# Optimization experiments

Measured on AMD Instinct MI355X. Metric: run time of the kernel, lower is better.

The kernel has to match this reference:

```python
import jax, jax.numpy as jnp
import numpy as np

N_CLUSTER = 1
SIZE, RATIO = 32, 0.1


def _lin_mat(n_in, n_out):
    # bilinear, align_corners=True interpolation matrix [n_out, n_in]
    src = np.arange(n_out) * (n_in - 1) / (n_out - 1)
    lo = np.floor(src).astype(np.int64)
    hi = np.minimum(lo + 1, n_in - 1)
    w = (src - lo).astype(np.float32)
    M = np.zeros((n_out, n_in), np.float32)
    M[np.arange(n_out), lo] += 1.0 - w
    M[np.arange(n_out), hi] += w
    return jnp.asarray(M)


def setup_inputs() -> dict:
    key = jax.random.key(0)
    ks = jax.random.split(key, 5)
    B, D, H, W, C = 16, 128, 128, 128, 6
    inp = {
        "assp": jax.random.normal(ks[0], (B, D, H, W), jnp.float32),
        "cls_w": jax.random.normal(ks[1], (C, D), jnp.float32) * 0.05,
        "cls_b": jnp.zeros((C,), jnp.float32),
        "key_w": jax.random.normal(ks[2], (128, D), jnp.float32) * 0.05,
        "key_b": jnp.zeros((128,), jnp.float32),
        "query_w": jax.random.normal(ks[3], (C, 128, D), jnp.float32) * 0.05,
        "query_b": jnp.zeros((C, 128), jnp.float32),
    }
    rng = np.random.default_rng(0)
    idx = rng.permutation(SIZE * SIZE)[: int(SIZE * SIZE * RATIO)]  # 102 unique pixels
    inp["px"] = jnp.asarray(idx // SIZE, jnp.int32)
    inp["py"] = jnp.asarray(idx % SIZE, jnp.int32)
    return inp


def reference(assp, cls_w, cls_b, key_w, key_b, query_w, query_b, px, py):
    B, D, H, W = assp.shape
    C = cls_w.shape[0]
    # pseudo labels (torch.no_grad)
    feats = jax.lax.stop_gradient(assp)
    pseudo = jnp.einsum('bdhw,cd->bchw', feats, cls_w) + cls_b[None, :, None, None]
    mask = jnp.argmax(pseudo, axis=1)                      # [B,H,W]
    onehot = jax.nn.one_hot(mask, C, dtype=assp.dtype)      # [B,H,W,C]
    counts = onehot.sum((1, 2))                             # [B,C]
    sums = jnp.einsum('bdhw,bhwc->bcd', assp, onehot)       # masked class sums
    protoC = sums / (counts[..., None] + 1e-5)              # [B,C,D]
    protoC = jnp.where(counts[..., None] > 0, protoC, 0.0)  # zero_prototype fallback
    protos12 = jnp.broadcast_to(protoC[:, :, None, :], (B, C, 2, D)).reshape(B, 2 * C, D)

    # DomainTrain: gather sampled pixels, L2 dist to 12 prototypes, argmin, scatter replace
    feat_px = assp[:, :, px, py]                            # [B,D,Np]
    diff = protos12[:, :, None, :] - feat_px.transpose(0, 2, 1)[:, None, :, :]  # [B,12,Np,D]
    dist = jnp.linalg.norm(diff, axis=-1)                   # [B,12,Np]
    closest = jnp.argmin(dist, axis=1)                      # [B,Np]
    repl = jnp.take_along_axis(protos12, closest[..., None], axis=1)  # [B,Np,D]
    assp = assp.at[:, :, px, py].set(repl.transpose(0, 2, 1))
    protos4 = protos12.reshape(B, C, 2, D)

    # key / query attention
    keymap = jnp.einsum('bdhw,kd->bkhw', assp, key_w) + key_b[None, :, None, None]
    q = jnp.einsum('bijd,ikd->bijk', protos4, query_w) + query_b[None, :, None, :]  # [B,C,2,128]
    sim = jnp.einsum('bijk,bkhw->bijhw', q, keymap).reshape(B, 2 * C, H, W)
    simw = jax.nn.softmax(sim / (2 * C) * N_CLUSTER, axis=1).mean(axis=1)  # [B,H,W]

    weighted = assp * simw[:, None]
    x = jnp.einsum('bdhw,cd->bchw', weighted, cls_w) + cls_b[None, :, None, None]
    My = _lin_mat(H, 4 * H)
    Mx = _lin_mat(W, 4 * W)
    xup = jnp.einsum('Hh,bchw,Ww->bcHW', My, x, Mx)
    return xup
```

## Files before the change

kernel.cpp:

```cpp
#include <hip/hip_runtime.h>

namespace {

constexpr int B  = 16;
constexpr int D  = 128;
constexpr int C  = 6;
constexpr int H  = 128;
constexpr int W  = 128;
constexpr int HWC = H * W;
constexpr int HO = 512, WO = 512;
constexpr int TILE = 64;
constexpr int TPB  = 8;

__global__ __launch_bounds__(256) void k_fused(const float* __restrict__ assp,
                                               const float* __restrict__ cls_w,
                                               const float* __restrict__ cls_b,
                                               float* __restrict__ sums,
                                               int* __restrict__ counts,
                                               float* __restrict__ x) {
  __shared__ float tile[D * TILE];
  __shared__ float red[4 * C * TILE];
  __shared__ float ws[C * D];
  __shared__ float bs[C];

  const int t  = threadIdx.x;
  const int b  = blockIdx.y;
  for (int i = t; i < C * D; i += 256) ws[i] = cls_w[i];
  if (t < C) bs[t] = cls_b[t];

  const int lane = t & 63;
  const int wv   = t >> 6;
  const int d2b  = t & 127;
  const int h2b  = t >> 7;
  const int d1   = t >> 5;
  const int px2  = (t & 31) * 2;

  float acc2b[C] = {0.f, 0.f, 0.f, 0.f, 0.f, 0.f};
  int   cnt_run  = 0;

  __syncthreads();

  for (int it = 0; it < TPB; ++it) {
    const int hw0 = (blockIdx.x * TPB + it) * TILE;
    const float* base = assp + ((size_t)b * D) * HWC + hw0;

    float2 v[16];
#pragma unroll
    for (int j = 0; j < 16; ++j) {
      int d = d1 + 8 * j;
      v[j] = *(const float2*)(base + (size_t)d * HWC + px2);
    }
#pragma unroll
    for (int j = 0; j < 16; ++j) {
      int d = d1 + 8 * j;
      *(float2*)&tile[d * TILE + (px2 ^ (d & 62))] = v[j];
    }
    __syncthreads();

    {
      float a[C] = {0.f, 0.f, 0.f, 0.f, 0.f, 0.f};
#pragma unroll
      for (int dd = 0; dd < 32; ++dd) {
        int d = wv * 32 + dd;
        float vv = tile[d * TILE + (lane ^ (d & 62))];
#pragma unroll
        for (int c = 0; c < C; ++c) a[c] += vv * ws[c * D + d];
      }
#pragma unroll
      for (int c = 0; c < C; ++c) red[(wv * C + c) * TILE + lane] = a[c];
    }
    __syncthreads();

    int cls;
    {
      float s[C];
#pragma unroll
      for (int c = 0; c < C; ++c)
        s[c] = red[(0 * C + c) * TILE + lane] + red[(1 * C + c) * TILE + lane]
             + red[(2 * C + c) * TILE + lane] + red[(3 * C + c) * TILE + lane];
      float bv = s[0] + bs[0]; cls = 0;
#pragma unroll
      for (int c = 1; c < C; ++c) {
        float pv = s[c] + bs[c];
        if (pv > bv) { bv = pv; cls = c; }
      }
      if (wv == 0) {
        const float inv12 = 1.0f / 12.0f;
        float* xb = x + ((size_t)b * C) * HWC + hw0 + lane;
#pragma unroll
        for (int c = 0; c < C; ++c) xb[(size_t)c * HWC] = s[c] * inv12 + bs[c];
#pragma unroll
        for (int c = 0; c < C; ++c) {
          unsigned long long m = __ballot(cls == c);
          if (lane == c) cnt_run += (int)__popcll(m);
        }
      }
    }

#pragma unroll
    for (int i = 0; i < 32; ++i) {
      int px = h2b * 32 + i;
      float vv = tile[d2b * TILE + (px ^ (d2b & 62))];
      int c = __shfl(cls, px, 64);
#pragma unroll
      for (int cc = 0; cc < C; ++cc) acc2b[cc] += (c == cc) ? vv : 0.f;
    }
    __syncthreads();
  }

  float* part = red;
  if (h2b == 1) {
#pragma unroll
    for (int c = 0; c < C; ++c) part[c * D + d2b] = acc2b[c];
  }
  __syncthreads();
  if (h2b == 0) {
#pragma unroll
    for (int c = 0; c < C; ++c) {
      float s = acc2b[c] + part[c * D + d2b];
      atomicAdd(&sums[((size_t)b * C + c) * D + d2b], s);
    }
  }
  if (wv == 0 && lane < C) atomicAdd(&counts[b * C + lane], cnt_run);
}

__global__ void k_patch(const float* __restrict__ assp,
                        const float* __restrict__ sums,
                        const int* __restrict__ counts,
                        const float* __restrict__ cls_w,
                        const float* __restrict__ cls_b,
                        const int* __restrict__ px,
                        const int* __restrict__ py,
                        int P,
                        float* __restrict__ x) {
  int bp = blockIdx.x;
  int b = bp / P, p = bp % P;
  int hw = px[p] * W + py[p];
  int lane = threadIdx.x;
  const float* fbase = assp + ((size_t)b * D) * HWC + hw;

  float f0 = fbase[(size_t)lane * HWC];
  float f1 = fbase[(size_t)(lane + 64) * HWC];

  float pv0[C], pv1[C], ds[C];
#pragma unroll
  for (int c = 0; c < C; ++c) {
    float cnt = (float)counts[b * C + c];
    float s0 = sums[((size_t)b * C + c) * D + lane];
    float s1 = sums[((size_t)b * C + c) * D + lane + 64];
    float q0 = (cnt > 0.f) ? s0 / (cnt + 1e-5f) : 0.f;
    float q1 = (cnt > 0.f) ? s1 / (cnt + 1e-5f) : 0.f;
    pv0[c] = q0; pv1[c] = q1;
    float e0 = q0 - f0, e1 = q1 - f1;
    float tt = e0 * e0 + e1 * e1;
#pragma unroll
    for (int off = 32; off >= 1; off >>= 1) tt += __shfl_xor(tt, off, 64);
    ds[c] = tt;
  }
  int best = 0; float bv = ds[0];
#pragma unroll
  for (int c = 1; c < C; ++c)
    if (ds[c] < bv) { bv = ds[c]; best = c; }

  float v0 = 0.f, v1 = 0.f;
#pragma unroll
  for (int c = 0; c < C; ++c) {
    if (best == c) { v0 = pv0[c]; v1 = pv1[c]; }
  }

  float myx = 0.f;
#pragma unroll
  for (int c = 0; c < C; ++c) {
    float tt = v0 * cls_w[c * D + lane] + v1 * cls_w[c * D + lane + 64];
#pragma unroll
    for (int off = 32; off >= 1; off >>= 1) tt += __shfl_xor(tt, off, 64);
    float val = tt * (1.0f / 12.0f) + cls_b[c];
    if (lane == c) myx = val;
  }
  if (lane < C) x[((size_t)b * C + lane) * HWC + hw] = myx;
}

__global__ void k_up(const float* __restrict__ x, float* __restrict__ out) {
  int t = blockIdx.x * 256 + threadIdx.x;
  int i = t * 4;
  int X  = i & (WO - 1);
  int Y  = (i >> 9) & (HO - 1);
  int bc = i >> 18;

  double sy = (double)(Y * (H - 1)) / (double)(HO - 1);
  int y0 = (int)sy;
  float wy = (float)(sy - (double)y0);
  int y1 = y0 + 1; if (y1 > H - 1) y1 = H - 1;

  const float* r0 = x + (size_t)bc * HWC + y0 * W;
  const float* r1 = x + (size_t)bc * HWC + y1 * W;

  float o[4];
#pragma unroll
  for (int j = 0; j < 4; ++j) {
    int Xj = X + j;
    double sx = (double)(Xj * (W - 1)) / (double)(WO - 1);
    int x0 = (int)sx;
    float wx = (float)(sx - (double)x0);
    int x1 = x0 + 1; if (x1 > W - 1) x1 = W - 1;

    float v00 = r0[x0], v01 = r0[x1], v10 = r1[x0], v11 = r1[x1];
    o[j] = (1.f - wy) * ((1.f - wx) * v00 + wx * v01)
         +        wy  * ((1.f - wx) * v10 + wx * v11);
  }
  float4 o4; o4.x = o[0]; o4.y = o[1]; o4.z = o[2]; o4.w = o[3];
  *(float4*)(out + i) = o4;
}

}

extern "C" void kernel_launch(void* const* d_in, const int* in_sizes, int n_in,
                              void* d_out, int out_size, void* d_ws, size_t ws_size,
                              hipStream_t stream) {
  const float* assp  = (const float*)d_in[0];
  const float* cls_w = (const float*)d_in[1];
  const float* cls_b = (const float*)d_in[2];
  const int*   px    = (const int*)d_in[7];
  const int*   py    = (const int*)d_in[8];
  const int    P     = in_sizes[7];

  char* ws = (char*)d_ws;
  float* sums   = (float*)ws;
  int*   counts = (int*)(ws + 49152);
  float* x      = (float*)(ws + 65536);

  float* out = (float*)d_out;

  hipMemsetAsync(ws, 0, 49152 + 384, stream);
  k_fused<<<dim3(HWC / (TILE * TPB), B), 256, 0, stream>>>(assp, cls_w, cls_b,
                                                           sums, counts, x);
  k_patch<<<B * P, 64, 0, stream>>>(assp, sums, counts, cls_w, cls_b, px, py, P, x);
  k_up<<<(B * C * HO * WO) / 1024, 256, 0, stream>>>(x, out);
}
```

Before: 276.9 us.

## Prefetch next tile in fused pass and stage upsample rows in LDS

The fused classification/sum kernel now issues global loads for the next 64-pixel tile into registers while it computes on the current one, and each block handles half as many tiles, doubling the grid. The upsample kernel loads the up to three source rows a block needs into shared memory with float4 reads. It replaces the double-precision divisions with integer index math, cutting redundant global reads and slow FP64 work. The cost is higher register pressure in the fused kernel from the prefetch buffers, plus twice as many atomic adds on the sums.

```diff
diff --git a/kernel.cpp b/kernel.cpp
--- a/kernel.cpp
+++ b/kernel.cpp
@@ -10,7 +10,7 @@
 constexpr int HWC = H * W;
 constexpr int HO = 512, WO = 512;
 constexpr int TILE = 64;
-constexpr int TPB  = 8;
+constexpr int TPB  = 4;
 
 __global__ __launch_bounds__(256) void k_fused(const float* __restrict__ assp,
                                                const float* __restrict__ cls_w,
@@ -38,24 +38,36 @@
   float acc2b[C] = {0.f, 0.f, 0.f, 0.f, 0.f, 0.f};
   int   cnt_run  = 0;
 
+  const int hw_base = blockIdx.x * (TILE * TPB);
+  const float* bbase = assp + ((size_t)b * D) * HWC + hw_base;
+
+  float2 v[16];
+#pragma unroll
+  for (int j = 0; j < 16; ++j) {
+    int d = d1 + 8 * j;
+    v[j] = *(const float2*)(bbase + (size_t)d * HWC + px2);
+  }
+
   __syncthreads();
 
   for (int it = 0; it < TPB; ++it) {
-    const int hw0 = (blockIdx.x * TPB + it) * TILE;
-    const float* base = assp + ((size_t)b * D) * HWC + hw0;
-
-    float2 v[16];
-#pragma unroll
-    for (int j = 0; j < 16; ++j) {
-      int d = d1 + 8 * j;
-      v[j] = *(const float2*)(base + (size_t)d * HWC + px2);
-    }
+    const int hw0 = hw_base + it * TILE;
+
 #pragma unroll
     for (int j = 0; j < 16; ++j) {
       int d = d1 + 8 * j;
       *(float2*)&tile[d * TILE + (px2 ^ (d & 62))] = v[j];
     }
     __syncthreads();
+
+    if (it + 1 < TPB) {
+      const float* nbase = bbase + (it + 1) * TILE;
+#pragma unroll
+      for (int j = 0; j < 16; ++j) {
+        int d = d1 + 8 * j;
+        v[j] = *(const float2*)(nbase + (size_t)d * HWC + px2);
+      }
+    }
 
     {
       float a[C] = {0.f, 0.f, 0.f, 0.f, 0.f, 0.f};
@@ -180,36 +192,52 @@
   if (lane < C) x[((size_t)b * C + lane) * HWC + hw] = myx;
 }
 
-__global__ void k_up(const float* __restrict__ x, float* __restrict__ out) {
-  int t = blockIdx.x * 256 + threadIdx.x;
-  int i = t * 4;
-  int X  = i & (WO - 1);
-  int Y  = (i >> 9) & (HO - 1);
-  int bc = i >> 18;
-
-  double sy = (double)(Y * (H - 1)) / (double)(HO - 1);
-  int y0 = (int)sy;
-  float wy = (float)(sy - (double)y0);
-  int y1 = y0 + 1; if (y1 > H - 1) y1 = H - 1;
-
-  const float* r0 = x + (size_t)bc * HWC + y0 * W;
-  const float* r1 = x + (size_t)bc * HWC + y1 * W;
+__global__ __launch_bounds__(256) void k_up(const float* __restrict__ x,
+                                            float* __restrict__ out) {
+  __shared__ float rows[3 * W];
+
+  const int t = threadIdx.x;
+  const size_t base = (size_t)blockIdx.x * 1024;
+  const int bc = (int)(base >> 18);
+  const int Y0 = ((int)(base >> 9)) & (HO - 1);
+
+  const int ry = (Y0 * (H - 1)) / (HO - 1);
+
+  if (t < 96) {
+    int r  = t >> 5;
+    int xx = (t & 31) * 4;
+    int rr = ry + r; if (rr > H - 1) rr = H - 1;
+    *(float4*)&rows[r * W + xx] =
+        *(const float4*)(x + (size_t)bc * HWC + (size_t)rr * W + xx);
+  }
+  __syncthreads();
+
+  const int h  = t >> 7;
+  const int tt = t & 127;
+  const int Y  = Y0 + h;
+
+  const int ynum = Y * (H - 1);
+  const int yl   = ynum / (HO - 1);
+  const float wy = (float)((double)(ynum - yl * (HO - 1)) * (1.0 / (HO - 1)));
+  int yh = yl + 1; if (yh > H - 1) yh = H - 1;
+  const float* r0 = &rows[(yl - ry) * W];
+  const float* r1 = &rows[(yh - ry) * W];
 
   float o[4];
 #pragma unroll
   for (int j = 0; j < 4; ++j) {
-    int Xj = X + j;
-    double sx = (double)(Xj * (W - 1)) / (double)(WO - 1);
-    int x0 = (int)sx;
-    float wx = (float)(sx - (double)x0);
-    int x1 = x0 + 1; if (x1 > W - 1) x1 = W - 1;
-
-    float v00 = r0[x0], v01 = r0[x1], v10 = r1[x0], v11 = r1[x1];
+    int X   = 4 * tt + j;
+    int num = X * (W - 1);
+    int lo  = num / (WO - 1);
+    float wx = (float)((double)(num - lo * (WO - 1)) * (1.0 / (WO - 1)));
+    int hi = lo + 1; if (hi > W - 1) hi = W - 1;
+
+    float v00 = r0[lo], v01 = r0[hi], v10 = r1[lo], v11 = r1[hi];
     o[j] = (1.f - wy) * ((1.f - wx) * v00 + wx * v01)
          +        wy  * ((1.f - wx) * v10 + wx * v11);
   }
-  float4 o4; o4.x = o[0]; o4.y = o[1]; o4.z = o[2]; o4.w = o[3];
-  *(float4*)(out + i) = o4;
+  float4 o4 = {o[0], o[1], o[2], o[3]};
+  *(float4*)(out + base + (size_t)h * WO + 4 * tt) = o4;
 }
 
 }
```

Result: faster. 268.9 us (-2.9%).
